# Kernel optimization log

Hardware: AMD Instinct MI355X
Metric: run time of the kernel (lower is better)

## Reference

```python
import jax, jax.numpy as jnp
import numpy as np
from jax import lax

D = 128      # d_model
NH = 8       # nhead
DIM = D // NH
B, H, W = 2, 160, 160
EPS_ATT = 1e-6


def setup_inputs() -> dict:
    key = jax.random.key(0)
    ks = iter(jax.random.split(key, 40))
    def n(*s):
        return jax.random.normal(next(ks), s, dtype=jnp.float32) * 0.05
    inp = {
        "x": jax.random.normal(next(ks), (B, D, H, W), jnp.float32),
        "source": jax.random.normal(next(ks), (B, D, H, W), jnp.float32),
        # q/k/v 1x1 conv (with bias)
        "wq": n(D, D), "bq": n(D),
        "wk": n(D, D), "bk": n(D),
        "wv": n(D, D), "bv": n(D),
        # multiscale aggregation (scale=5): depthwise 5x5 (no bias) + pointwise 1x1 (no bias)
        "dwq": n(D, 1, 5, 5), "pwq": n(D, D),
        "dwk": n(D, 1, 5, 5), "pwk": n(D, D),
        "dwv": n(D, 1, 5, 5), "pwv": n(D, D),
        # attention output projection: 2*d_model -> d_model, no bias
        "wproj": n(D, 2 * D),
        # merge 1x1 conv
        "wmerge": n(D, D), "bmerge": n(D),
        # conv ffn: d -> 2d -> d
        "wff1": n(2 * D, D), "bff1": n(2 * D),
        "wff2": n(D, 2 * D), "bff2": n(D),
        # layernorms over channel dim
        "ln1_w": 1.0 + n(D), "ln1_b": n(D),
        "ln2_w": 1.0 + n(D), "ln2_b": n(D),
    }
    return inp


def _pw(t, Wm, b=None):
    # 1x1 conv as channel matmul; t: [B,C,H,W], Wm: [O,C]
    y = jnp.einsum('bchw,oc->bohw', t, Wm)
    return y if b is None else y + b[None, :, None, None]


def _bn(t):
    # BatchNorm2d, training-mode batch stats, affine=False, eps=1e-5
    m = t.mean((0, 2, 3), keepdims=True)
    v = t.var((0, 2, 3), keepdims=True)
    return (t - m) * lax.rsqrt(v + 1e-5)


def _gelu(t):
    return jax.nn.gelu(t, approximate=False)


def _dw(t, Wk):
    # depthwise 5x5 conv, stride 1, SAME padding (== padding=2)
    return lax.conv_general_dilated(t, Wk, (1, 1), 'SAME',
                                    dimension_numbers=('NCHW', 'OIHW', 'NCHW'),
                                    feature_group_count=D)


def _ln(t, w, b):
    # LayerNorm over channel axis of NCHW tensor, eps=1e-5
    m = t.mean(1, keepdims=True)
    v = t.var(1, keepdims=True)
    return (t - m) * lax.rsqrt(v + 1e-5) * w[None, :, None, None] + b[None, :, None, None]


def reference(x, source, wq, bq, wk, bk, wv, bv, dwq, pwq, dwk, pwk, dwv, pwv,
              wproj, wmerge, bmerge, wff1, bff1, wff2, bff2,
              ln1_w, ln1_b, ln2_w, ln2_b):
    q = _gelu(_bn(_pw(x, wq, bq)))
    k = _gelu(_bn(_pw(source, wk, bk)))
    v = _gelu(_bn(_pw(source, wv, bv)))

    # multiscale aggregation: concat original with one scale-5 depthwise+pointwise branch
    qc = jnp.concatenate([q, _pw(_dw(q, dwq), pwq)], axis=1)
    kc = jnp.concatenate([k, _pw(_dw(k, dwk), pwk)], axis=1)
    vc = jnp.concatenate([v, _pw(_dw(v, dwv), pwv)], axis=1)

    qc = jax.nn.relu(qc)  # kernel feature map
    kc = jax.nn.relu(kc)

    b_, C2, h1, w1 = qc.shape           # C2 = 2*d_model
    h2, w2 = kc.shape[2], kc.shape[3]
    L1, L2 = h1 * w1, h2 * w2
    H2 = C2 // DIM                       # effective heads = 2*nhead

    qf = qc.reshape(b_, C2, L1).transpose(0, 2, 1).reshape(b_, L1, H2, DIM)
    kf = kc.reshape(b_, C2, L2).transpose(0, 2, 1).reshape(b_, L2, H2, DIM)
    vf = vc.reshape(b_, C2, L2).transpose(0, 2, 1).reshape(b_, L2, H2, DIM)

    vf = vf / L2
    kv = jnp.einsum('nshd,nshv->nhdv', kf, vf)                       # [b,H2,d,d]
    z = 1.0 / jnp.maximum(jnp.einsum('nlhd,nhd->nlh', qf, kf.sum(1) / L2), EPS_ATT)
    qv = jnp.einsum('nlhd,nhdv,nlh->nlhv', qf, kv, z)                # [b,L1,H2,d]

    out = qv.transpose(0, 2, 3, 1).reshape(b_, C2, h1, w1)
    msg = _pw(out, wproj)                                            # 2d -> d

    msg = _gelu(_bn(_pw(msg, wmerge, bmerge)))
    msg = x + msg
    msg = _ln(msg, ln1_w, ln1_b)

    ff = _gelu(_bn(_pw(msg, wff1, bff1)))
    ff = _gelu(_bn(_pw(ff, wff2, bff2)))
    return _ln(ff + msg, ln2_w, ln2_b)
```

## Files before the change

### kernel.cpp

```cpp
#include <hip/hip_runtime.h>
#include <math.h>

#define LL 25600
#define NTOTF 51200.f
#define NSH 8

using f16   = _Float16;
using f16x8 = __attribute__((ext_vector_type(8))) _Float16;
using f16x4 = __attribute__((ext_vector_type(4))) _Float16;
using f16x2 = __attribute__((ext_vector_type(2))) _Float16;
using f32x4 = __attribute__((ext_vector_type(4))) float;

__device__ __forceinline__ float gelu_f(float v) {
    const float u2 = v * (1.5957691216057308f + 0.0713548162726009f * v * v);
    const float e  = __expf(u2);
    return v * (1.f - 1.f / (e + 1.f));
}

__device__ __forceinline__ void stat_mr(const float* st, int C, int c,
                                        float& m, float& r) {
    float s1 = 0.f, s2 = 0.f;
#pragma unroll
    for (int sh = 0; sh < NSH; ++sh) {
        s1 += st[sh * 2 * C + c];
        s2 += st[sh * 2 * C + C + c];
    }
    m = s1 * (1.f / NTOTF);
    r = rsqrtf(s2 * (1.f / NTOTF) - m * m + 1e-5f);
}

template <int M, int K, int PP, int NSEG, bool IN32, bool LDG, bool TWOW,
          bool BIAS, bool STATS>
__global__ __launch_bounds__(512, 2) void gemm_kernel(
    const void* __restrict__ X1, const void* __restrict__ X2,
    const void* __restrict__ X3,
    const float* __restrict__ WA, const float* __restrict__ WB,
    const float* __restrict__ W2, const float* __restrict__ W3,
    const float* __restrict__ biasA, const float* __restrict__ biasB,
    const float* __restrict__ lstat,
    f16* __restrict__ Y1, f16* __restrict__ Y2, f16* __restrict__ Y3,
    float* __restrict__ ostat)
{
    constexpr int MR  = M / 128;
    constexpr int KS  = K / 32;
    constexpr int NR  = PP / 16;
    constexpr int PG  = PP / 8;
    constexpr int NCH = (K * PG) / 512;
    constexpr int NCHUNK = LL / PP;

    __shared__ f16 Xs[PP * K];

    const int tid  = threadIdx.x;
    const int lane = tid & 63;
    const int wv   = tid >> 6;
    const int lm16 = lane & 15, lg = lane >> 4;
    const int row0 = wv * (M / 8);

    int bx = blockIdx.x, seg = 0;
    if (NSEG > 1) { seg = bx / (2 * NCHUNK); bx -= seg * 2 * NCHUNK; }
    const int bb  = bx / NCHUNK;
    const int pp0 = (bx - bb * NCHUNK) * PP;

    const void*  Xp = (NSEG > 1) ? (seg == 0 ? X1 : (seg == 1 ? X2 : X3)) : X1;
    const float* Wp = (NSEG > 1) ? (seg == 0 ? WA : (seg == 1 ? W2 : W3)) : WA;
    f16*         Yp = (NSEG > 1) ? (seg == 0 ? Y1 : (seg == 1 ? Y2 : Y3)) : Y1;

    const int c0  = (tid / PG) * NCH;
    const int p0g = (tid % PG) * 8;

    f16x8 xin[NCH];
#pragma unroll
    for (int cc = 0; cc < NCH; ++cc) {
        const size_t roff = (size_t)(bb * K + c0 + cc) * LL + pp0 + p0g;
        if (IN32) {
            const float4 a  = *reinterpret_cast<const float4*>(
                                  reinterpret_cast<const float*>(Xp) + roff);
            const float4 b2 = *reinterpret_cast<const float4*>(
                                  reinterpret_cast<const float*>(Xp) + roff + 4);
            f16x8 v;
            v[0] = (f16)a.x;  v[1] = (f16)a.y;  v[2] = (f16)a.z;  v[3] = (f16)a.w;
            v[4] = (f16)b2.x; v[5] = (f16)b2.y; v[6] = (f16)b2.z; v[7] = (f16)b2.w;
            xin[cc] = v;
        } else {
            xin[cc] = *reinterpret_cast<const f16x8*>(
                          reinterpret_cast<const f16*>(Xp) + roff);
        }
    }

    f16x8 wfr[KS][MR];
#pragma unroll
    for (int k = 0; k < KS; ++k) {
        const int col = k * 32 + lg * 8;
#pragma unroll
        for (int mr = 0; mr < MR; ++mr) {
            const int row = row0 + mr * 16 + lm16;
            const float* wp = (TWOW && row >= 128)
                                  ? WB + (size_t)(row - 128) * K + col
                                  : Wp + (size_t)row * K + col;
            const float4 wa = *reinterpret_cast<const float4*>(wp);
            const float4 wb2 = *reinterpret_cast<const float4*>(wp + 4);
            f16x8 v;
            v[0] = (f16)wa.x; v[1] = (f16)wa.y; v[2] = (f16)wa.z; v[3] = (f16)wa.w;
            v[4] = (f16)wb2.x; v[5] = (f16)wb2.y; v[6] = (f16)wb2.z; v[7] = (f16)wb2.w;
            wfr[k][mr] = v;
        }
    }

    float bvv[MR], st1[MR], st2[MR];
#pragma unroll
    for (int mr = 0; mr < MR; ++mr) {
        const int o = row0 + mr * 16 + lm16;
        bvv[mr] = BIAS ? ((TWOW && o >= 128) ? biasB[o - 128] : biasA[o]) : 0.f;
        st1[mr] = 0.f; st2[mr] = 0.f;
    }

    if (LDG) {
#pragma unroll
        for (int cc = 0; cc < NCH; ++cc) {
            const int c = c0 + cc;
            float m, r;
            stat_mr(lstat, K, c, m, r);
#pragma unroll
            for (int j = 0; j < 8; ++j)
                xin[cc][j] = (f16)gelu_f(((float)xin[cc][j] - m) * r);
        }
    }

#pragma unroll
    for (int j = 0; j < 8; ++j) {
        const int pos = p0g + j;
        const int swz = ((pos & 7) ^ ((pos >> 3) & 7)) << 3;
        if constexpr (NCH == 8) {
            f16x8 v;
#pragma unroll
            for (int cc = 0; cc < 8; ++cc) v[cc] = xin[cc][j];
            *reinterpret_cast<f16x8*>(&Xs[(size_t)pos * K + (c0 ^ swz)]) = v;
        } else if constexpr (NCH == 4) {
            f16x4 v;
#pragma unroll
            for (int cc = 0; cc < 4; ++cc) v[cc] = xin[cc][j];
            *reinterpret_cast<f16x4*>(&Xs[(size_t)pos * K + (c0 ^ swz)]) = v;
        } else {
            f16x2 v;
#pragma unroll
            for (int cc = 0; cc < 2; ++cc) v[cc] = xin[cc][j];
            *reinterpret_cast<f16x2*>(&Xs[(size_t)pos * K + (c0 ^ swz)]) = v;
        }
    }
    __syncthreads();

    f32x4 acc[MR][NR];
#pragma unroll
    for (int mr = 0; mr < MR; ++mr)
#pragma unroll
        for (int nr = 0; nr < NR; ++nr)
            acc[mr][nr] = (f32x4){0.f, 0.f, 0.f, 0.f};

#pragma unroll
    for (int k = 0; k < KS; ++k) {
        const int kc = k * 32 + lg * 8;
        f16x8 xa[NR];
#pragma unroll
        for (int nr = 0; nr < NR; ++nr) {
            const int pos = nr * 16 + lm16;
            const int swz = ((pos & 7) ^ ((pos >> 3) & 7)) << 3;
            xa[nr] = *reinterpret_cast<const f16x8*>(
                &Xs[(size_t)pos * K + (kc ^ swz)]);
        }
#pragma unroll
        for (int mr = 0; mr < MR; ++mr)
#pragma unroll
            for (int nr = 0; nr < NR; ++nr)
                acc[mr][nr] = __builtin_amdgcn_mfma_f32_16x16x32_f16(
                    xa[nr], wfr[k][mr], acc[mr][nr], 0, 0, 0);
    }

#pragma unroll
    for (int mr = 0; mr < MR; ++mr) {
        const int o = row0 + mr * 16 + lm16;
        f16* yb = Yp + (size_t)(bb * M + o) * LL + pp0;
#pragma unroll
        for (int nr = 0; nr < NR; ++nr) {
            f16x4 o4;
#pragma unroll
            for (int r = 0; r < 4; ++r) {
                const float v = acc[mr][nr][r] + bvv[mr];
                o4[r] = (f16)v;
                if (STATS) { st1[mr] += v; st2[mr] += v * v; }
            }
            *reinterpret_cast<f16x4*>(yb + nr * 16 + lg * 4) = o4;
        }
    }

    if (STATS) {
        float* osb = ostat + (size_t)(blockIdx.x & (NSH - 1)) * 2 * M;
#pragma unroll
        for (int mr = 0; mr < MR; ++mr) {
            float s1 = st1[mr], s2 = st2[mr];
            s1 += __shfl_xor(s1, 16); s2 += __shfl_xor(s2, 16);
            s1 += __shfl_xor(s1, 32); s2 += __shfl_xor(s2, 32);
            if (lane < 16) {
                const int o = row0 + mr * 16 + lm16;
                atomicAdd(&osb[o], s1);
                atomicAdd(&osb[M + o], s2);
            }
        }
    }
}

__global__ __launch_bounds__(256) void act_kernel(
    const f16* __restrict__ qraw, const f16* __restrict__ kvraw,
    const float* __restrict__ sQ, const float* __restrict__ sKV,
    f16* __restrict__ actq, f16* __restrict__ actkv)
{
    const int idx = blockIdx.x * 256 + threadIdx.x;
    const f16* src; f16* dst; const float* st; int C, local;
    if (idx < 819200) { src = qraw;  dst = actq;  st = sQ;  C = 128; local = idx; }
    else              { src = kvraw; dst = actkv; st = sKV; C = 256; local = idx - 819200; }
    const int c = (local / 3200) % C;
    float m, r;
    stat_mr(st, C, c, m, r);
    const f16x8 v = *reinterpret_cast<const f16x8*>(src + (size_t)local * 8);
    f16x8 o;
#pragma unroll
    for (int j = 0; j < 8; ++j)
        o[j] = (f16)gelu_f(((float)v[j] - m) * r);
    *reinterpret_cast<f16x8*>(dst + (size_t)local * 8) = o;
}

__global__ __launch_bounds__(256) void dw5_kernel(
    const f16* __restrict__ actq, const f16* __restrict__ actkv,
    const float* __restrict__ dwq, const float* __restrict__ dwk,
    const float* __restrict__ dwv,
    f16* __restrict__ oq, f16* __restrict__ ok, f16* __restrict__ ov)
{
    __shared__ f16x2 pt[20][41];
    const int z = blockIdx.z;
    const int which = z >> 8;
    const int bc = z & 255;
    const int b = bc >> 7, c = bc & 127;

    const f16* src; const float* wdwp; f16* outp;
    if (which == 0)      { src = actq  + (size_t)(b * 128 + c) * LL;       wdwp = dwq + c * 25; outp = oq; }
    else if (which == 1) { src = actkv + (size_t)(b * 256 + c) * LL;       wdwp = dwk + c * 25; outp = ok; }
    else                 { src = actkv + (size_t)(b * 256 + 128 + c) * LL; wdwp = dwv + c * 25; outp = ov; }

    const int h0 = blockIdx.y * 32, w0 = blockIdx.x * 32;
    const int tid = threadIdx.x;

    f16x2 wp[25];
#pragma unroll
    for (int q = 0; q < 25; ++q) {
        const f16 wv16 = (f16)wdwp[q];
        wp[q][0] = wv16; wp[q][1] = wv16;
    }

    for (int idx = tid; idx < 720; idx += 256) {
        const int t  = idx / 36, cc = idx - t * 36;
        const int iw = w0 - 2 + cc;
        const int ih0 = h0 - 2 + t, ih1 = ih0 + 16;
        const int iwc  = min(max(iw, 0), 159);
        const int ihc0 = min(max(ih0, 0), 159);
        const int ihc1 = min(max(ih1, 0), 159);
        const bool okw = (iw >= 0) & (iw < 160);
        f16 lo = src[ihc0 * 160 + iwc];
        f16 hi = src[ihc1 * 160 + iwc];
        if (!(okw & (ih0 >= 0) & (ih0 < 160))) lo = (f16)0;
        if (!(okw & (ih1 >= 0) & (ih1 < 160))) hi = (f16)0;
        f16x2 pv; pv[0] = lo; pv[1] = hi;
        pt[t][cc] = pv;
    }
    __syncthreads();

    const int ylo = tid >> 4, xq = tid & 15, x0 = xq * 2;

    f16x2 a0; a0[0] = (f16)0; a0[1] = (f16)0;
    f16x2 a1 = a0;
#pragma unroll
    for (int u = 0; u < 5; ++u) {
        const f16x2* row = &pt[ylo + u][x0];
        const f16x2 r0 = row[0], r1 = row[1], r2 = row[2];
        const f16x2 r3 = row[3], r4 = row[4], r5 = row[5];
        a0 += wp[u*5+0] * r0;  a1 += wp[u*5+0] * r1;
        a0 += wp[u*5+1] * r1;  a1 += wp[u*5+1] * r2;
        a0 += wp[u*5+2] * r2;  a1 += wp[u*5+2] * r3;
        a0 += wp[u*5+3] * r3;  a1 += wp[u*5+3] * r4;
        a0 += wp[u*5+4] * r4;  a1 += wp[u*5+4] * r5;
    }

    f16* ob = outp + (size_t)(b * 128 + c) * LL + (size_t)(h0 + ylo) * 160 + (w0 + x0);
    f16x2 lo2; lo2[0] = a0[0]; lo2[1] = a1[0];
    f16x2 hi2; hi2[0] = a0[1]; hi2[1] = a1[1];
    *reinterpret_cast<f16x2*>(ob) = lo2;
    *reinterpret_cast<f16x2*>(ob + 16 * 160) = hi2;
}

__global__ __launch_bounds__(256) void att_reduce_kernel(
    const f16* __restrict__ ACT, const f16* __restrict__ K2,
    const f16* __restrict__ V2,
    float* __restrict__ kvout, float* __restrict__ ksum)
{
    __shared__ float kvred[4][256];

    const int bx = blockIdx.x;
    const int b = bx / 400;
    const int rem = bx - b * 400;
    const int h = rem / 25;
    const int chunk = rem - h * 25;
    const int tid = threadIdx.x;
    const int wv = tid >> 6, l = tid & 63;
    const int ch = l & 15, kg = l >> 4;
    const bool half1 = h < 8;

    const f16* kbase = half1 ? ACT + (size_t)(b * 256 + h * 16 + ch) * LL
                             : K2 + (size_t)(b * 128 + (h - 8) * 16 + ch) * LL;
    const f16* vbase = half1 ? ACT + (size_t)(b * 256 + 128 + h * 16 + ch) * LL
                             : V2 + (size_t)(b * 128 + (h - 8) * 16 + ch) * LL;

    f32x4 acc = (f32x4){0.f, 0.f, 0.f, 0.f};
    float ksacc = 0.f;
    const int base = chunk * 1024 + kg * 8;
#pragma unroll
    for (int it = 0; it < 8; ++it) {
        const int p = base + wv * 256 + it * 32;
        const f16x8 kf = *reinterpret_cast<const f16x8*>(kbase + p);
        const f16x8 vf = *reinterpret_cast<const f16x8*>(vbase + p);
        f16x8 ka;
#pragma unroll
        for (int j = 0; j < 8; ++j) {
            const f16 kv_ = kf[j];
            ka[j] = (kv_ > (f16)0) ? kv_ : (f16)0;
            ksacc += (float)ka[j];
        }
        acc = __builtin_amdgcn_mfma_f32_16x16x32_f16(ka, vf, acc, 0, 0, 0);
    }

    constexpr float s = 1.f / (float)LL;
#pragma unroll
    for (int r = 0; r < 4; ++r)
        kvred[wv][(kg * 4 + r) * 16 + ch] = acc[r];
    __syncthreads();
    {
        float t = kvred[0][tid] + kvred[1][tid] + kvred[2][tid] + kvred[3][tid];
        atomicAdd(&kvout[(size_t)(b * 16 + h) * 256 + tid], t * s);
    }

    float s1 = ksacc;
    s1 += __shfl_xor(s1, 16);
    s1 += __shfl_xor(s1, 32);
    if (l < 16) atomicAdd(&ksum[(size_t)(b * 16 + h) * 16 + ch], s1 * s);
}

__global__ __launch_bounds__(256) void att_apply_kernel(
    const f16* __restrict__ Q, const f16* __restrict__ Q2,
    const float* __restrict__ kvin, const float* __restrict__ ksumin,
    f16* __restrict__ att)
{
    __shared__ float kvs[256];
    __shared__ float kss[16];

    const int bx = blockIdx.x;
    const int b = bx / 1600;
    const int rem = bx - b * 1600;
    const int h = rem / 100;
    const int chunk = rem - h * 100;
    const int tid = threadIdx.x;
    const int p = chunk * 256 + tid;

    kvs[tid] = kvin[(size_t)b * 4096 + h * 256 + tid];
    if (tid < 16) kss[tid] = ksumin[(size_t)b * 256 + h * 16 + tid];
    __syncthreads();

    const f16* qb = (h < 8) ? Q + (size_t)(b * 128 + h * 16) * LL
                            : Q2 + (size_t)(b * 128 + (h - 8) * 16) * LL;
    float s[16];
#pragma unroll
    for (int d = 0; d < 16; ++d)
        s[d] = fmaxf((float)qb[(size_t)d * LL + p], 0.f);
    float denom = 0.f;
#pragma unroll
    for (int d = 0; d < 16; ++d) denom = fmaf(s[d], kss[d], denom);
    const float z = 1.f / fmaxf(denom, 1e-6f);

    f16* ob = att + (size_t)(b * 256 + h * 16) * LL + p;
#pragma unroll
    for (int e = 0; e < 16; ++e) {
        float acc = 0.f;
#pragma unroll
        for (int d = 0; d < 16; ++d)
            acc = fmaf(s[d], kvs[d * 16 + e], acc);
        ob[(size_t)e * LL] = (f16)(acc * z);
    }
}

template <bool RES32, bool OUT32>
__global__ __launch_bounds__(256) void fuse_ln_kernel(
    const f16* __restrict__ yconv, const void* __restrict__ residv,
    const float* __restrict__ stat,
    const float* __restrict__ lnw, const float* __restrict__ lnb,
    void* __restrict__ outv)
{
    __shared__ float t[128][65];
    __shared__ float mrs[128][2];
    __shared__ float red[4][64][2];
    __shared__ float mln[64], rln[64];

    const int bx = blockIdx.x;
    const int b = bx / 400, p0 = (bx - b * 400) * 64;
    const int tid = threadIdx.x;

    if (tid < 128) {
        float m, r;
        stat_mr(stat, 128, tid, m, r);
        mrs[tid][0] = m; mrs[tid][1] = r;
    }
    __syncthreads();

#pragma unroll
    for (int it = 0; it < 4; ++it) {
        const int chunk = it * 256 + tid;
        const int c  = chunk >> 3;
        const int pg = (chunk & 7) * 8;
        const size_t off = (size_t)(b * 128 + c) * LL + p0 + pg;
        const f16x8 yv = *reinterpret_cast<const f16x8*>(yconv + off);
        const float m = mrs[c][0], r = mrs[c][1];
        float rv[8];
        if (RES32) {
            const float* rp = reinterpret_cast<const float*>(residv) + off;
            const float4 ra = *reinterpret_cast<const float4*>(rp);
            const float4 rb = *reinterpret_cast<const float4*>(rp + 4);
            rv[0] = ra.x; rv[1] = ra.y; rv[2] = ra.z; rv[3] = ra.w;
            rv[4] = rb.x; rv[5] = rb.y; rv[6] = rb.z; rv[7] = rb.w;
        } else {
            const f16x8 rr = *reinterpret_cast<const f16x8*>(
                reinterpret_cast<const f16*>(residv) + off);
#pragma unroll
            for (int j = 0; j < 8; ++j) rv[j] = (float)rr[j];
        }
#pragma unroll
        for (int j = 0; j < 8; ++j)
            t[c][pg + j] = gelu_f(((float)yv[j] - m) * r) + rv[j];
    }
    __syncthreads();

    {
        const int i = tid & 63, q = tid >> 6;
        float ps = 0.f, pq = 0.f;
        for (int c = q * 32; c < q * 32 + 32; ++c) {
            const float v = t[c][i];
            ps += v; pq += v * v;
        }
        red[q][i][0] = ps; red[q][i][1] = pq;
    }
    __syncthreads();
    if (tid < 64) {
        float s1 = 0.f, s2 = 0.f;
#pragma unroll
        for (int q = 0; q < 4; ++q) { s1 += red[q][tid][0]; s2 += red[q][tid][1]; }
        const float m = s1 * (1.f / 128.f);
        const float var = s2 * (1.f / 128.f) - m * m;
        mln[tid] = m; rln[tid] = rsqrtf(var + 1e-5f);
    }
    __syncthreads();

#pragma unroll
    for (int it = 0; it < 4; ++it) {
        const int chunk = it * 256 + tid;
        const int c  = chunk >> 3;
        const int pg = (chunk & 7) * 8;
        const size_t off = (size_t)(b * 128 + c) * LL + p0 + pg;
        const float lw = lnw[c], lb = lnb[c];
        if (OUT32) {
            float4 oa, ob2;
            float* op = reinterpret_cast<float*>(outv) + off;
            oa.x = (t[c][pg+0] - mln[pg+0]) * rln[pg+0] * lw + lb;
            oa.y = (t[c][pg+1] - mln[pg+1]) * rln[pg+1] * lw + lb;
            oa.z = (t[c][pg+2] - mln[pg+2]) * rln[pg+2] * lw + lb;
            oa.w = (t[c][pg+3] - mln[pg+3]) * rln[pg+3] * lw + lb;
            ob2.x = (t[c][pg+4] - mln[pg+4]) * rln[pg+4] * lw + lb;
            ob2.y = (t[c][pg+5] - mln[pg+5]) * rln[pg+5] * lw + lb;
            ob2.z = (t[c][pg+6] - mln[pg+6]) * rln[pg+6] * lw + lb;
            ob2.w = (t[c][pg+7] - mln[pg+7]) * rln[pg+7] * lw + lb;
            *reinterpret_cast<float4*>(op) = oa;
            *reinterpret_cast<float4*>(op + 4) = ob2;
        } else {
            f16x8 o;
#pragma unroll
            for (int j = 0; j < 8; ++j)
                o[j] = (f16)((t[c][pg + j] - mln[pg + j]) * rln[pg + j] * lw + lb);
            *reinterpret_cast<f16x8*>(reinterpret_cast<f16*>(outv) + off) = o;
        }
    }
}

__global__ __launch_bounds__(256) void wcomb_kernel(
    const float* __restrict__ wmerge, const float* __restrict__ wproj,
    float* __restrict__ wc)
{
    const int o = blockIdx.x;
    const int c2 = threadIdx.x;
    float acc = 0.f;
#pragma unroll 4
    for (int m = 0; m < 128; ++m)
        acc = fmaf(wmerge[o * 128 + m], wproj[m * 256 + c2], acc);
    wc[o * 256 + c2] = acc;
}

extern "C" void kernel_launch(void* const* d_in, const int* in_sizes, int n_in,
                              void* d_out, int out_size, void* d_ws, size_t ws_size,
                              hipStream_t stream)
{
    const float* x      = (const float*)d_in[0];
    const float* source = (const float*)d_in[1];
    const float* wq = (const float*)d_in[2];  const float* bq = (const float*)d_in[3];
    const float* wk = (const float*)d_in[4];  const float* bk = (const float*)d_in[5];
    const float* wvw = (const float*)d_in[6]; const float* bvb = (const float*)d_in[7];
    const float* dwq = (const float*)d_in[8];  const float* pwq = (const float*)d_in[9];
    const float* dwk = (const float*)d_in[10]; const float* pwk = (const float*)d_in[11];
    const float* dwv = (const float*)d_in[12]; const float* pwv = (const float*)d_in[13];
    const float* wproj  = (const float*)d_in[14];
    const float* wmerge = (const float*)d_in[15]; const float* bmerge = (const float*)d_in[16];
    const float* wff1 = (const float*)d_in[17]; const float* bff1 = (const float*)d_in[18];
    const float* wff2 = (const float*)d_in[19]; const float* bff2 = (const float*)d_in[20];
    const float* ln1w = (const float*)d_in[21]; const float* ln1b = (const float*)d_in[22];
    const float* ln2w = (const float*)d_in[23]; const float* ln2b = (const float*)d_in[24];

    const size_t UNIT  = (size_t)2 * 128 * LL;
    const size_t UNITB = UNIT * sizeof(f16);
    char* w = (char*)d_ws;
    f16* qraw  = (f16*)w; w += UNITB;
    f16* kvraw = (f16*)w; w += 2 * UNITB;
    f16* actq  = (f16*)w; w += UNITB;
    f16* actkv = (f16*)w; w += 2 * UNITB;
    f16* q2raw = (f16*)w; w += UNITB;
    f16* k2raw = (f16*)w; w += UNITB;
    f16* v2raw = (f16*)w; w += UNITB;
    f16* y2raw = (f16*)w; w += UNITB;
    f16* msg   = (f16*)w; w += UNITB;
    f16* ff1raw= (f16*)w; w += 2 * UNITB;
    f16* ff2raw= (f16*)w; w += UNITB;

    f16* dtq = qraw;
    f16* dtk = kvraw;
    f16* dtv = kvraw + UNIT;
    f16* att = actkv;

    float* zbase = (float*)w;
    float* kvred = zbase;
    float* ksum  = zbase + 8192;
    float* sQ    = zbase + 8704;
    float* sKV   = sQ + NSH * 256;
    float* sM    = sKV + NSH * 512;
    float* sF1   = sM + NSH * 256;
    float* sF2   = sF1 + NSH * 512;
    const size_t zcount = 8192 + 512 + NSH * (256 + 512 + 256 + 512 + 256);
    float* wcomb = zbase + zcount;

    hipMemsetAsync(zbase, 0, zcount * sizeof(float), stream);
    wcomb_kernel<<<128, 256, 0, stream>>>(wmerge, wproj, wcomb);

    gemm_kernel<128,128,128,1,true,false,false,true,true><<<400, 512, 0, stream>>>(
        x, nullptr, nullptr, wq, nullptr, nullptr, nullptr, bq, nullptr, nullptr,
        qraw, nullptr, nullptr, sQ);
    gemm_kernel<256,128,64,1,true,false,true,true,true><<<800, 512, 0, stream>>>(
        source, nullptr, nullptr, wk, wvw, nullptr, nullptr, bk, bvb, nullptr,
        kvraw, nullptr, nullptr, sKV);

    act_kernel<<<9600, 256, 0, stream>>>(qraw, kvraw, sQ, sKV, actq, actkv);

    dim3 dwg(5, 5, 768);
    dw5_kernel<<<dwg, 256, 0, stream>>>(actq, actkv, dwq, dwk, dwv, dtq, dtk, dtv);
    gemm_kernel<128,128,128,3,false,false,false,false,false><<<1200, 512, 0, stream>>>(
        dtq, dtk, dtv, pwq, nullptr, pwk, pwv, nullptr, nullptr, nullptr,
        q2raw, k2raw, v2raw, nullptr);

    att_reduce_kernel<<<800, 256, 0, stream>>>(actkv, k2raw, v2raw, kvred, ksum);
    att_apply_kernel<<<3200, 256, 0, stream>>>(actq, q2raw, kvred, ksum, att);

    gemm_kernel<128,256,128,1,false,false,false,true,true><<<400, 512, 0, stream>>>(
        att, nullptr, nullptr, wcomb, nullptr, nullptr, nullptr, bmerge, nullptr,
        nullptr, y2raw, nullptr, nullptr, sM);

    fuse_ln_kernel<true,false><<<800, 256, 0, stream>>>(
        y2raw, x, sM, ln1w, ln1b, msg);

    gemm_kernel<256,128,64,1,false,false,false,true,true><<<800, 512, 0, stream>>>(
        msg, nullptr, nullptr, wff1, nullptr, nullptr, nullptr, bff1, nullptr,
        nullptr, ff1raw, nullptr, nullptr, sF1);
    gemm_kernel<128,256,128,1,false,true,false,true,true><<<400, 512, 0, stream>>>(
        ff1raw, nullptr, nullptr, wff2, nullptr, nullptr, nullptr, bff2, nullptr,
        sF1, ff2raw, nullptr, nullptr, sF2);

    fuse_ln_kernel<false,true><<<800, 256, 0, stream>>>(
        ff2raw, msg, sF2, ln2w, ln2b, (float*)d_out);
}
```

Measured before the change: 258.5 us.

## Fuse BN+GELU activation into depthwise conv and attention consumers, drop act kernel

Removes the standalone activation kernel that normalized and GELU'd the q/k/v projections into separate buffers. The depthwise conv, attention reduce and attention apply kernels now read the raw projections and apply the batch-stat normalization and GELU on the fly. This eliminates a full write and read of three activation tensors, at the cost of recomputing GELU in each consumer (the conv tile includes halo recomputation). The zeroing memset is also folded into the weight-combine kernel to save a launch, and the workspace layout is changed so the conv outputs no longer alias the raw buffers.

```diff
diff --git a/kernel.cpp b/kernel.cpp
--- a/kernel.cpp
+++ b/kernel.cpp
@@ -208,28 +208,9 @@
     }
 }
 
-__global__ __launch_bounds__(256) void act_kernel(
+__global__ __launch_bounds__(256) void dw5_kernel(
     const f16* __restrict__ qraw, const f16* __restrict__ kvraw,
     const float* __restrict__ sQ, const float* __restrict__ sKV,
-    f16* __restrict__ actq, f16* __restrict__ actkv)
-{
-    const int idx = blockIdx.x * 256 + threadIdx.x;
-    const f16* src; f16* dst; const float* st; int C, local;
-    if (idx < 819200) { src = qraw;  dst = actq;  st = sQ;  C = 128; local = idx; }
-    else              { src = kvraw; dst = actkv; st = sKV; C = 256; local = idx - 819200; }
-    const int c = (local / 3200) % C;
-    float m, r;
-    stat_mr(st, C, c, m, r);
-    const f16x8 v = *reinterpret_cast<const f16x8*>(src + (size_t)local * 8);
-    f16x8 o;
-#pragma unroll
-    for (int j = 0; j < 8; ++j)
-        o[j] = (f16)gelu_f(((float)v[j] - m) * r);
-    *reinterpret_cast<f16x8*>(dst + (size_t)local * 8) = o;
-}
-
-__global__ __launch_bounds__(256) void dw5_kernel(
-    const f16* __restrict__ actq, const f16* __restrict__ actkv,
     const float* __restrict__ dwq, const float* __restrict__ dwk,
     const float* __restrict__ dwv,
     f16* __restrict__ oq, f16* __restrict__ ok, f16* __restrict__ ov)
@@ -241,9 +222,16 @@
     const int b = bc >> 7, c = bc & 127;
 
     const f16* src; const float* wdwp; f16* outp;
-    if (which == 0)      { src = actq  + (size_t)(b * 128 + c) * LL;       wdwp = dwq + c * 25; outp = oq; }
-    else if (which == 1) { src = actkv + (size_t)(b * 256 + c) * LL;       wdwp = dwk + c * 25; outp = ok; }
-    else                 { src = actkv + (size_t)(b * 256 + 128 + c) * LL; wdwp = dwv + c * 25; outp = ov; }
+    float m, r;
+    if (which == 0)      { src = qraw  + (size_t)(b * 128 + c) * LL;
+                           wdwp = dwq + c * 25; outp = oq;
+                           stat_mr(sQ, 128, c, m, r); }
+    else if (which == 1) { src = kvraw + (size_t)(b * 256 + c) * LL;
+                           wdwp = dwk + c * 25; outp = ok;
+                           stat_mr(sKV, 256, c, m, r); }
+    else                 { src = kvraw + (size_t)(b * 256 + 128 + c) * LL;
+                           wdwp = dwv + c * 25; outp = ov;
+                           stat_mr(sKV, 256, 128 + c, m, r); }
 
     const int h0 = blockIdx.y * 32, w0 = blockIdx.x * 32;
     const int tid = threadIdx.x;
@@ -263,11 +251,11 @@
         const int ihc0 = min(max(ih0, 0), 159);
         const int ihc1 = min(max(ih1, 0), 159);
         const bool okw = (iw >= 0) & (iw < 160);
-        f16 lo = src[ihc0 * 160 + iwc];
-        f16 hi = src[ihc1 * 160 + iwc];
-        if (!(okw & (ih0 >= 0) & (ih0 < 160))) lo = (f16)0;
-        if (!(okw & (ih1 >= 0) & (ih1 < 160))) hi = (f16)0;
-        f16x2 pv; pv[0] = lo; pv[1] = hi;
+        float lo = gelu_f(((float)src[ihc0 * 160 + iwc] - m) * r);
+        float hi = gelu_f(((float)src[ihc1 * 160 + iwc] - m) * r);
+        if (!(okw & (ih0 >= 0) & (ih0 < 160))) lo = 0.f;
+        if (!(okw & (ih1 >= 0) & (ih1 < 160))) hi = 0.f;
+        f16x2 pv; pv[0] = (f16)lo; pv[1] = (f16)hi;
         pt[t][cc] = pv;
     }
     __syncthreads();
@@ -296,8 +284,8 @@
 }
 
 __global__ __launch_bounds__(256) void att_reduce_kernel(
-    const f16* __restrict__ ACT, const f16* __restrict__ K2,
-    const f16* __restrict__ V2,
+    const f16* __restrict__ KVRAW, const f16* __restrict__ K2,
+    const f16* __restrict__ V2, const float* __restrict__ sKV,
     float* __restrict__ kvout, float* __restrict__ ksum)
 {
     __shared__ float kvred[4][256];
@@ -312,9 +300,15 @@
     const int ch = l & 15, kg = l >> 4;
     const bool half1 = h < 8;
 
-    const f16* kbase = half1 ? ACT + (size_t)(b * 256 + h * 16 + ch) * LL
+    float mk = 0.f, rk = 1.f, mv = 0.f, rv = 1.f;
+    if (half1) {
+        stat_mr(sKV, 256, h * 16 + ch, mk, rk);
+        stat_mr(sKV, 256, 128 + h * 16 + ch, mv, rv);
+    }
+
+    const f16* kbase = half1 ? KVRAW + (size_t)(b * 256 + h * 16 + ch) * LL
                              : K2 + (size_t)(b * 128 + (h - 8) * 16 + ch) * LL;
-    const f16* vbase = half1 ? ACT + (size_t)(b * 256 + 128 + h * 16 + ch) * LL
+    const f16* vbase = half1 ? KVRAW + (size_t)(b * 256 + 128 + h * 16 + ch) * LL
                              : V2 + (size_t)(b * 128 + (h - 8) * 16 + ch) * LL;
 
     f32x4 acc = (f32x4){0.f, 0.f, 0.f, 0.f};
@@ -325,14 +319,19 @@
         const int p = base + wv * 256 + it * 32;
         const f16x8 kf = *reinterpret_cast<const f16x8*>(kbase + p);
         const f16x8 vf = *reinterpret_cast<const f16x8*>(vbase + p);
-        f16x8 ka;
+        f16x8 ka, vb;
 #pragma unroll
         for (int j = 0; j < 8; ++j) {
-            const f16 kv_ = kf[j];
-            ka[j] = (kv_ > (f16)0) ? kv_ : (f16)0;
-            ksacc += (float)ka[j];
-        }
-        acc = __builtin_amdgcn_mfma_f32_16x16x32_f16(ka, vf, acc, 0, 0, 0);
+            float kl = (float)kf[j];
+            if (half1) kl = gelu_f((kl - mk) * rk);
+            kl = fmaxf(kl, 0.f);
+            ksacc += kl;
+            ka[j] = (f16)kl;
+            float vl = (float)vf[j];
+            if (half1) vl = gelu_f((vl - mv) * rv);
+            vb[j] = (f16)vl;
+        }
+        acc = __builtin_amdgcn_mfma_f32_16x16x32_f16(ka, vb, acc, 0, 0, 0);
     }
 
     constexpr float s = 1.f / (float)LL;
@@ -352,12 +351,14 @@
 }
 
 __global__ __launch_bounds__(256) void att_apply_kernel(
-    const f16* __restrict__ Q, const f16* __restrict__ Q2,
+    const f16* __restrict__ QRAW, const f16* __restrict__ Q2,
+    const float* __restrict__ sQ,
     const float* __restrict__ kvin, const float* __restrict__ ksumin,
     f16* __restrict__ att)
 {
     __shared__ float kvs[256];
     __shared__ float kss[16];
+    __shared__ float mq[16], rq[16];
 
     const int bx = blockIdx.x;
     const int b = bx / 1600;
@@ -368,15 +369,25 @@
     const int p = chunk * 256 + tid;
 
     kvs[tid] = kvin[(size_t)b * 4096 + h * 256 + tid];
-    if (tid < 16) kss[tid] = ksumin[(size_t)b * 256 + h * 16 + tid];
-    __syncthreads();
-
-    const f16* qb = (h < 8) ? Q + (size_t)(b * 128 + h * 16) * LL
+    if (tid < 16) {
+        kss[tid] = ksumin[(size_t)b * 256 + h * 16 + tid];
+        if (h < 8) {
+            float m, r;
+            stat_mr(sQ, 128, h * 16 + tid, m, r);
+            mq[tid] = m; rq[tid] = r;
+        } else { mq[tid] = 0.f; rq[tid] = 1.f; }
+    }
+    __syncthreads();
+
+    const f16* qb = (h < 8) ? QRAW + (size_t)(b * 128 + h * 16) * LL
                             : Q2 + (size_t)(b * 128 + (h - 8) * 16) * LL;
     float s[16];
 #pragma unroll
-    for (int d = 0; d < 16; ++d)
-        s[d] = fmaxf((float)qb[(size_t)d * LL + p], 0.f);
+    for (int d = 0; d < 16; ++d) {
+        float v = (float)qb[(size_t)d * LL + p];
+        if (h < 8) v = gelu_f((v - mq[d]) * rq[d]);
+        s[d] = fmaxf(v, 0.f);
+    }
     float denom = 0.f;
 #pragma unroll
     for (int d = 0; d < 16; ++d) denom = fmaf(s[d], kss[d], denom);
@@ -495,8 +506,11 @@
 
 __global__ __launch_bounds__(256) void wcomb_kernel(
     const float* __restrict__ wmerge, const float* __restrict__ wproj,
-    float* __restrict__ wc)
+    float* __restrict__ wc, float* __restrict__ zbase, int zcount)
 {
+    const int g = blockIdx.x * 256 + threadIdx.x;
+    if (g < zcount) zbase[g] = 0.f;
+
     const int o = blockIdx.x;
     const int c2 = threadIdx.x;
     float acc = 0.f;
@@ -530,20 +544,17 @@
     char* w = (char*)d_ws;
     f16* qraw  = (f16*)w; w += UNITB;
     f16* kvraw = (f16*)w; w += 2 * UNITB;
-    f16* actq  = (f16*)w; w += UNITB;
-    f16* actkv = (f16*)w; w += 2 * UNITB;
+    f16* dtq   = (f16*)w; w += UNITB;
+    f16* dtk   = (f16*)w; w += UNITB;
+    f16* dtv   = (f16*)w; w += UNITB;
     f16* q2raw = (f16*)w; w += UNITB;
     f16* k2raw = (f16*)w; w += UNITB;
     f16* v2raw = (f16*)w; w += UNITB;
+    f16* att   = (f16*)w; w += 2 * UNITB;
     f16* y2raw = (f16*)w; w += UNITB;
     f16* msg   = (f16*)w; w += UNITB;
     f16* ff1raw= (f16*)w; w += 2 * UNITB;
     f16* ff2raw= (f16*)w; w += UNITB;
-
-    f16* dtq = qraw;
-    f16* dtk = kvraw;
-    f16* dtv = kvraw + UNIT;
-    f16* att = actkv;
 
     float* zbase = (float*)w;
     float* kvred = zbase;
@@ -553,11 +564,10 @@
     float* sM    = sKV + NSH * 512;
     float* sF1   = sM + NSH * 256;
     float* sF2   = sF1 + NSH * 512;
-    const size_t zcount = 8192 + 512 + NSH * (256 + 512 + 256 + 512 + 256);
+    const int zcount = 8192 + 512 + NSH * (256 + 512 + 256 + 512 + 256);
     float* wcomb = zbase + zcount;
 
-    hipMemsetAsync(zbase, 0, zcount * sizeof(float), stream);
-    wcomb_kernel<<<128, 256, 0, stream>>>(wmerge, wproj, wcomb);
+    wcomb_kernel<<<128, 256, 0, stream>>>(wmerge, wproj, wcomb, zbase, zcount);
 
     gemm_kernel<128,128,128,1,true,false,false,true,true><<<400, 512, 0, stream>>>(
         x, nullptr, nullptr, wq, nullptr, nullptr, nullptr, bq, nullptr, nullptr,
@@ -566,16 +576,15 @@
         source, nullptr, nullptr, wk, wvw, nullptr, nullptr, bk, bvb, nullptr,
         kvraw, nullptr, nullptr, sKV);
 
-    act_kernel<<<9600, 256, 0, stream>>>(qraw, kvraw, sQ, sKV, actq, actkv);
-
     dim3 dwg(5, 5, 768);
-    dw5_kernel<<<dwg, 256, 0, stream>>>(actq, actkv, dwq, dwk, dwv, dtq, dtk, dtv);
+    dw5_kernel<<<dwg, 256, 0, stream>>>(qraw, kvraw, sQ, sKV, dwq, dwk, dwv,
+                                        dtq, dtk, dtv);
     gemm_kernel<128,128,128,3,false,false,false,false,false><<<1200, 512, 0, stream>>>(
         dtq, dtk, dtv, pwq, nullptr, pwk, pwv, nullptr, nullptr, nullptr,
         q2raw, k2raw, v2raw, nullptr);
 
-    att_reduce_kernel<<<800, 256, 0, stream>>>(actkv, k2raw, v2raw, kvred, ksum);
-    att_apply_kernel<<<3200, 256, 0, stream>>>(actq, q2raw, kvred, ksum, att);
+    att_reduce_kernel<<<800, 256, 0, stream>>>(kvraw, k2raw, v2raw, sKV, kvred, ksum);
+    att_apply_kernel<<<3200, 256, 0, stream>>>(qraw, q2raw, sQ, kvred, ksum, att);
 
     gemm_kernel<128,256,128,1,false,false,false,true,true><<<400, 512, 0, stream>>>(
         att, nullptr, nullptr, wcomb, nullptr, nullptr, nullptr, bmerge, nullptr,
```

Result: slower. 274.8 us (+6.3%).

## Retile depthwise conv to full-width row strips and fold memset into wcomb

Applied to the files above, without the earlier changes.

The depthwise 5x5 kernel now processes full 160-wide rows in 8-row strips instead of 32x32 tiles. Rows are loaded with vectorized f16x2 reads, explicit zero halos are written, and each thread computes 5 outputs in fp32 FMA, which removes the column clamping and per-element gather. Separately, the hipMemsetAsync that zeroed the reduction buffers is dropped and the zeroing is done inside wcomb_kernel, saving one launch. The trade-offs are that the new halo covers 12 rows for every 8 output rows, and the output stores are scalar f16 writes at stride 5, which may coalesce poorly. The memset folding is only correct because every zcount element is covered by the 128x256 threads of wcomb and the kernels that accumulate into these buffers run later in the stream.

```diff
diff --git a/kernel.cpp b/kernel.cpp
--- a/kernel.cpp
+++ b/kernel.cpp
@@ -234,7 +234,7 @@
     const float* __restrict__ dwv,
     f16* __restrict__ oq, f16* __restrict__ ok, f16* __restrict__ ov)
 {
-    __shared__ f16x2 pt[20][41];
+    __shared__ f16 pt[12][164];
     const int z = blockIdx.z;
     const int which = z >> 8;
     const int bc = z & 255;
@@ -245,54 +245,50 @@
     else if (which == 1) { src = actkv + (size_t)(b * 256 + c) * LL;       wdwp = dwk + c * 25; outp = ok; }
     else                 { src = actkv + (size_t)(b * 256 + 128 + c) * LL; wdwp = dwv + c * 25; outp = ov; }
 
-    const int h0 = blockIdx.y * 32, w0 = blockIdx.x * 32;
+    const int h0 = blockIdx.y * 8;
     const int tid = threadIdx.x;
 
-    f16x2 wp[25];
-#pragma unroll
-    for (int q = 0; q < 25; ++q) {
-        const f16 wv16 = (f16)wdwp[q];
-        wp[q][0] = wv16; wp[q][1] = wv16;
-    }
-
-    for (int idx = tid; idx < 720; idx += 256) {
-        const int t  = idx / 36, cc = idx - t * 36;
-        const int iw = w0 - 2 + cc;
-        const int ih0 = h0 - 2 + t, ih1 = ih0 + 16;
-        const int iwc  = min(max(iw, 0), 159);
-        const int ihc0 = min(max(ih0, 0), 159);
-        const int ihc1 = min(max(ih1, 0), 159);
-        const bool okw = (iw >= 0) & (iw < 160);
-        f16 lo = src[ihc0 * 160 + iwc];
-        f16 hi = src[ihc1 * 160 + iwc];
-        if (!(okw & (ih0 >= 0) & (ih0 < 160))) lo = (f16)0;
-        if (!(okw & (ih1 >= 0) & (ih1 < 160))) hi = (f16)0;
-        f16x2 pv; pv[0] = lo; pv[1] = hi;
-        pt[t][cc] = pv;
-    }
-    __syncthreads();
-
-    const int ylo = tid >> 4, xq = tid & 15, x0 = xq * 2;
-
-    f16x2 a0; a0[0] = (f16)0; a0[1] = (f16)0;
-    f16x2 a1 = a0;
+    float wr[25];
+#pragma unroll
+    for (int q = 0; q < 25; ++q) wr[q] = wdwp[q];
+
+    if (tid < 48) {
+        const int t = tid >> 2, k = tid & 3;
+        pt[t][(k < 2) ? k : 160 + k] = (f16)0;
+    }
+    for (int idx = tid; idx < 960; idx += 256) {
+        const int t = idx / 80, j = idx - t * 80;
+        const int ih = h0 - 2 + t;
+        f16x2 v;
+        if (ih >= 0 && ih < 160)
+            v = *reinterpret_cast<const f16x2*>(src + ih * 160 + j * 2);
+        else { v[0] = (f16)0; v[1] = (f16)0; }
+        *reinterpret_cast<f16x2*>(&pt[t][2 + j * 2]) = v;
+    }
+    __syncthreads();
+
+    const int y  = tid >> 5;
+    const int x0 = (tid & 31) * 5;
+
+    float acc[5] = {0.f, 0.f, 0.f, 0.f, 0.f};
 #pragma unroll
     for (int u = 0; u < 5; ++u) {
-        const f16x2* row = &pt[ylo + u][x0];
-        const f16x2 r0 = row[0], r1 = row[1], r2 = row[2];
-        const f16x2 r3 = row[3], r4 = row[4], r5 = row[5];
-        a0 += wp[u*5+0] * r0;  a1 += wp[u*5+0] * r1;
-        a0 += wp[u*5+1] * r1;  a1 += wp[u*5+1] * r2;
-        a0 += wp[u*5+2] * r2;  a1 += wp[u*5+2] * r3;
-        a0 += wp[u*5+3] * r3;  a1 += wp[u*5+3] * r4;
-        a0 += wp[u*5+4] * r4;  a1 += wp[u*5+4] * r5;
-    }
-
-    f16* ob = outp + (size_t)(b * 128 + c) * LL + (size_t)(h0 + ylo) * 160 + (w0 + x0);
-    f16x2 lo2; lo2[0] = a0[0]; lo2[1] = a1[0];
-    f16x2 hi2; hi2[0] = a0[1]; hi2[1] = a1[1];
-    *reinterpret_cast<f16x2*>(ob) = lo2;
-    *reinterpret_cast<f16x2*>(ob + 16 * 160) = hi2;
+        const f16* row = &pt[y + u][x0];
+        float r[9];
+#pragma unroll
+        for (int j = 0; j < 9; ++j) r[j] = (float)row[j];
+#pragma unroll
+        for (int v = 0; v < 5; ++v) {
+            const float wv = wr[u * 5 + v];
+#pragma unroll
+            for (int i = 0; i < 5; ++i)
+                acc[i] = fmaf(wv, r[v + i], acc[i]);
+        }
+    }
+
+    f16* ob = outp + (size_t)(b * 128 + c) * LL + (size_t)(h0 + y) * 160 + x0;
+#pragma unroll
+    for (int i = 0; i < 5; ++i) ob[i] = (f16)acc[i];
 }
 
 __global__ __launch_bounds__(256) void att_reduce_kernel(
@@ -495,8 +491,11 @@
 
 __global__ __launch_bounds__(256) void wcomb_kernel(
     const float* __restrict__ wmerge, const float* __restrict__ wproj,
-    float* __restrict__ wc)
-{
+    float* __restrict__ wc, float* __restrict__ zbase, int zcount)
+{
+    const int g = blockIdx.x * 256 + threadIdx.x;
+    if (g < zcount) zbase[g] = 0.f;
+
     const int o = blockIdx.x;
     const int c2 = threadIdx.x;
     float acc = 0.f;
@@ -553,11 +552,10 @@
     float* sM    = sKV + NSH * 512;
     float* sF1   = sM + NSH * 256;
     float* sF2   = sF1 + NSH * 512;
-    const size_t zcount = 8192 + 512 + NSH * (256 + 512 + 256 + 512 + 256);
+    const int zcount = 8192 + 512 + NSH * (256 + 512 + 256 + 512 + 256);
     float* wcomb = zbase + zcount;
 
-    hipMemsetAsync(zbase, 0, zcount * sizeof(float), stream);
-    wcomb_kernel<<<128, 256, 0, stream>>>(wmerge, wproj, wcomb);
+    wcomb_kernel<<<128, 256, 0, stream>>>(wmerge, wproj, wcomb, zbase, zcount);
 
     gemm_kernel<128,128,128,1,true,false,false,true,true><<<400, 512, 0, stream>>>(
         x, nullptr, nullptr, wq, nullptr, nullptr, nullptr, bq, nullptr, nullptr,
@@ -568,7 +566,7 @@
 
     act_kernel<<<9600, 256, 0, stream>>>(qraw, kvraw, sQ, sKV, actq, actkv);
 
-    dim3 dwg(5, 5, 768);
+    dim3 dwg(1, 20, 768);
     dw5_kernel<<<dwg, 256, 0, stream>>>(actq, actkv, dwq, dwk, dwv, dtq, dtk, dtv);
     gemm_kernel<128,128,128,3,false,false,false,false,false><<<1200, 512, 0, stream>>>(
         dtq, dtk, dtv, pwq, nullptr, pwk, pwv, nullptr, nullptr, nullptr,
```

Result: slower. 373.8 us (+44.6%).
